# Kernel optimization log

Hardware: AMD Instinct MI355X
Metric: run time of the kernel (lower is better)

Reference implementation:

```python
import jax, jax.numpy as jnp
import numpy as np

A, B, NB = 100_000, 200_000, 6      # atoms, directed bonds, max neighbors
FA, FB, H = 133, 147, 256            # atom fdim, bond fdim, hidden
M, DEPTH = 5_000, 4                  # molecules, message-passing depth


def setup_inputs() -> dict:
    key = jax.random.key(0)
    ks = jax.random.split(key, 12)
    f_atoms = jax.random.normal(ks[0], (A, FA), jnp.float32)
    f_bonds = jax.random.normal(ks[1], (B, FB), jnp.float32)
    a2b = jax.random.randint(ks[2], (A, NB), 0, B, dtype=jnp.int32)
    b2a = jax.random.randint(ks[3], (B,), 0, A, dtype=jnp.int32)
    b2revb = jax.random.randint(ks[4], (B,), 0, B, dtype=jnp.int32)
    # weights (bias=False per args.bias, except W_o which always has bias)
    W_ia = jax.random.normal(ks[5], (FA, H), jnp.float32) / np.sqrt(FA)
    W_ib = jax.random.normal(ks[6], (FB, H), jnp.float32) / np.sqrt(FB)
    W_h = jax.random.normal(ks[7], (DEPTH - 1, H, H), jnp.float32) / np.sqrt(H)
    W_o = jax.random.normal(ks[8], (H, H), jnp.float32) / np.sqrt(H)
    b_o = jax.random.normal(ks[9], (H,), jnp.float32) * 0.01
    W_lr = jax.random.normal(ks[10], (3 * H, H), jnp.float32) / np.sqrt(3 * H)
    # ragged molecule sizes summing exactly to A (avg 20 atoms/mol)
    rng = np.random.default_rng(0)
    sizes = (A // M) + rng.integers(-5, 6, M)
    sizes[-1] += A - sizes.sum()
    sizes = jnp.asarray(sizes, jnp.int32)
    return dict(f_atoms=f_atoms, f_bonds=f_bonds, W_ia=W_ia, W_ib=W_ib,
                W_h=W_h, W_o=W_o, b_o=b_o, W_lr=W_lr,
                a2b=a2b, b2a=b2a, b2revb=b2revb, sizes=sizes)


def _sum_max_agg(message_bond, a2b):
    nei = message_bond[a2b]                 # [A, NB, H] gather
    return nei.sum(axis=1) * nei.max(axis=1)


def reference(f_atoms, f_bonds, W_ia, W_ib, W_h, W_o, b_o, W_lr,
              a2b, b2a, b2revb, sizes):
    input_atom = jax.nn.relu(f_atoms @ W_ia)    # [A, H]
    message_atom = input_atom
    input_bond = jax.nn.relu(f_bonds @ W_ib)    # [B, H]
    message_bond = input_bond
    for d in range(DEPTH - 1):
        agg = _sum_max_agg(message_bond, a2b)          # [A, H]
        message_atom = message_atom + agg
        rev = message_bond[b2revb]                     # [B, H]
        message_bond = message_atom[b2a] - rev
        message_bond = jax.nn.relu(input_bond + message_bond @ W_h[d])
        # dropout p=0.0 -> identity
    agg = _sum_max_agg(message_bond, a2b)              # [A, H]
    agg = jnp.concatenate([agg, message_atom, input_atom], axis=1) @ W_lr
    atom_hiddens = jax.nn.relu(agg @ W_o + b_o)        # [A, H]
    # ragged per-molecule mean pooling (a_scope)
    mol_ids = jnp.repeat(jnp.arange(M), sizes, total_repeat_length=A)
    sums = jax.ops.segment_sum(atom_hiddens, mol_ids, num_segments=M)
    mol_vecs = sums / sizes[:, None].astype(atom_hiddens.dtype)
    return mol_vecs                                    # [M, H]
```

## Files before the change

kernel.cpp:

```cpp
#include <hip/hip_runtime.h>


typedef _Float16 f16;
typedef f16 f16x4 __attribute__((ext_vector_type(4)));
typedef __attribute__((ext_vector_type(8))) short bh8;
typedef __attribute__((ext_vector_type(4))) float f32x4;

#define MB_SCALE 0.000244140625f
#define MB_INV   4096.0f
#define AGG_INV  16777216.0f

__device__ __forceinline__ unsigned short f2bf_rne(float f) {
    unsigned u = __float_as_uint(f);
    unsigned r = (u + 0x7fffu + ((u >> 16) & 1u)) >> 16;
    return (unsigned short)r;
}
__device__ __forceinline__ float bfu2f(unsigned short u) {
    return __uint_as_float(((unsigned)u) << 16);
}
__device__ __forceinline__ f32x4 mfma16(bh8 a, bh8 b, f32x4 c) {
    return __builtin_amdgcn_mfma_f32_16x16x32_bf16(a, b, c, 0, 0, 0);
}

__global__ __launch_bounds__(256) void wprep_kernel(
    const float* __restrict__ Wia, const float* __restrict__ Wib,
    const float* __restrict__ Wh,  const float* __restrict__ Wlr,
    const float* __restrict__ Wo,  short* __restrict__ ws)
{
    short* WiaT_hi = ws;
    short* WiaT_lo = ws + 40960;
    short* WibT_hi = ws + 81920;
    short* WibT_lo = ws + 122880;
    short* WhT_hi  = ws + 163840;
    short* WhT_lo  = ws + 360448;
    short* WlrT_hi = ws + 557056;
    short* WlrT_lo = ws + 753664;
    short* WoT_hi  = ws + 950272;
    short* WoT_lo  = ws + 1015808;

    int idx = blockIdx.x * 256 + threadIdx.x;
    float v; short *ph, *pl; int o;
    if (idx < 40960) {
        int n = idx / 160, k = idx - n * 160;
        v = (k < 133) ? Wia[(size_t)k * 256 + n] : 0.f;
        ph = WiaT_hi; pl = WiaT_lo; o = idx;
    } else if (idx < 81920) {
        int j = idx - 40960;
        int n = j / 160, k = j - n * 160;
        v = (k < 147) ? Wib[(size_t)k * 256 + n] : 0.f;
        ph = WibT_hi; pl = WibT_lo; o = j;
    } else if (idx < 278528) {
        int j = idx - 81920;
        int d = j >> 16, rem = j & 65535, n = rem >> 8, k = rem & 255;
        v = Wh[(size_t)d * 65536 + (size_t)k * 256 + n];
        ph = WhT_hi; pl = WhT_lo; o = j;
    } else if (idx < 475136) {
        int j = idx - 278528;
        int n = j / 768, k = j - n * 768;
        v = Wlr[(size_t)k * 256 + n];
        ph = WlrT_hi; pl = WlrT_lo; o = j;
    } else if (idx < 540672) {
        int j = idx - 475136;
        int n = j >> 8, k = j & 255;
        v = Wo[(size_t)k * 256 + n];
        ph = WoT_hi; pl = WoT_lo; o = j;
    } else return;
    unsigned short hb = f2bf_rne(v);
    ph[o] = (short)hb;
    pl[o] = (short)f2bf_rne(v - bfu2f(hb));
}

template <int KPAD, int SRC, int EPI>
__global__ __launch_bounds__(256) void mfma_gemm(
    const void* __restrict__ a0, const void* __restrict__ a1,
    const void* __restrict__ a2,
    const short* __restrict__ Bhi, const short* __restrict__ Blo,
    const float* __restrict__ bias, void* __restrict__ outv,
    int M, int Kact)
{
    __shared__ short As_hi[128 * 40];
    __shared__ short As_lo[(SRC == 2) ? 8 : 128 * 40];

    const int tid  = threadIdx.x;
    const int lane = tid & 63;
    const int w    = tid >> 6;
    const int wm   = (w >> 1) * 64;
    const int wn   = (w & 1) * 64;
    const int row0 = blockIdx.x * 128;
    const int colb = blockIdx.y * 128;

    const int sm = tid >> 1;
    const int sk = (tid & 1) * 16;
    const int fm = lane & 15;
    const int fk = (lane >> 4) * 8;

    int grow = row0 + sm; if (grow > M - 1) grow = M - 1;

    f32x4 acc[4][4];
#pragma unroll
    for (int i = 0; i < 4; ++i)
#pragma unroll
        for (int j = 0; j < 4; ++j) {
            f32x4 z = {0.f, 0.f, 0.f, 0.f};
            acc[i][j] = z;
        }

    for (int k0 = 0; k0 < KPAD; k0 += 32) {
        __syncthreads();
        if (SRC == 0) {
            const float* xrow = (const float*)a0 + (size_t)grow * Kact;
            bh8 h0, h1, l0, l1;
#pragma unroll
            for (int j = 0; j < 8; ++j) {
                int kc = k0 + sk + j;
                float v = (kc < Kact) ? xrow[kc] : 0.f;
                unsigned short hb = f2bf_rne(v);
                h0[j] = (short)hb; l0[j] = (short)f2bf_rne(v - bfu2f(hb));
                int kc2 = kc + 8;
                float v2 = (kc2 < Kact) ? xrow[kc2] : 0.f;
                unsigned short hb2 = f2bf_rne(v2);
                h1[j] = (short)hb2; l1[j] = (short)f2bf_rne(v2 - bfu2f(hb2));
            }
            int base = sm * 40 + sk;
            *(bh8*)&As_hi[base] = h0; *(bh8*)&As_hi[base + 8] = h1;
            *(bh8*)&As_lo[base] = l0; *(bh8*)&As_lo[base + 8] = l1;
        } else if (SRC == 1) {
            int base = sm * 40 + sk;
            if (k0 < 512) {
                const float* src = (k0 < 256) ? (const float*)a0 : (const float*)a1;
                int kl = k0 & 255;
                const float4* p = (const float4*)(src + (size_t)grow * 256 + kl + sk);
                float va[16];
#pragma unroll
                for (int q = 0; q < 4; ++q) {
                    float4 f = p[q];
                    va[q * 4 + 0] = f.x; va[q * 4 + 1] = f.y;
                    va[q * 4 + 2] = f.z; va[q * 4 + 3] = f.w;
                }
                bh8 h0, h1, l0, l1;
#pragma unroll
                for (int j = 0; j < 8; ++j) {
                    unsigned short hb = f2bf_rne(va[j]);
                    h0[j] = (short)hb; l0[j] = (short)f2bf_rne(va[j] - bfu2f(hb));
                    unsigned short hb2 = f2bf_rne(va[8 + j]);
                    h1[j] = (short)hb2; l1[j] = (short)f2bf_rne(va[8 + j] - bfu2f(hb2));
                }
                *(bh8*)&As_hi[base] = h0; *(bh8*)&As_hi[base + 8] = h1;
                *(bh8*)&As_lo[base] = l0; *(bh8*)&As_lo[base + 8] = l1;
            } else {
                const short* ia = (const short*)a2 + (size_t)grow * 256 + (k0 - 512) + sk;
                bh8 z;
#pragma unroll
                for (int j = 0; j < 8; ++j) z[j] = 0;
                *(bh8*)&As_hi[base]     = *(const bh8*)ia;
                *(bh8*)&As_hi[base + 8] = *(const bh8*)(ia + 8);
                *(bh8*)&As_lo[base] = z; *(bh8*)&As_lo[base + 8] = z;
            }
        } else {
            const short* xr = (const short*)a0 + (size_t)grow * 256 + k0 + sk;
            int base = sm * 40 + sk;
            *(bh8*)&As_hi[base]     = *(const bh8*)xr;
            *(bh8*)&As_hi[base + 8] = *(const bh8*)(xr + 8);
        }
        __syncthreads();

        bh8 bhf[4], blf[4];
#pragma unroll
        for (int nt = 0; nt < 4; ++nt) {
            int n = colb + wn + nt * 16 + fm;
            size_t off = (size_t)n * KPAD + k0 + fk;
            bhf[nt] = *(const bh8*)(Bhi + off);
            blf[nt] = *(const bh8*)(Blo + off);
        }
#pragma unroll
        for (int mt = 0; mt < 4; ++mt) {
            int abase = (wm + mt * 16 + fm) * 40 + fk;
            bh8 ah = *(const bh8*)&As_hi[abase];
#pragma unroll
            for (int nt = 0; nt < 4; ++nt) {
                acc[mt][nt] = mfma16(ah, bhf[nt], acc[mt][nt]);
                acc[mt][nt] = mfma16(ah, blf[nt], acc[mt][nt]);
            }
            if (SRC != 2) {
                bh8 al = *(const bh8*)&As_lo[abase];
#pragma unroll
                for (int nt = 0; nt < 4; ++nt)
                    acc[mt][nt] = mfma16(al, bhf[nt], acc[mt][nt]);
            }
        }
    }

#pragma unroll
    for (int mt = 0; mt < 4; ++mt) {
        int rbase = row0 + wm + mt * 16 + (lane >> 4) * 4;
#pragma unroll
        for (int nt = 0; nt < 4; ++nt) {
            int col = colb + wn + nt * 16 + fm;
            float bc = (EPI == 4) ? bias[col] : 0.f;
#pragma unroll
            for (int r = 0; r < 4; ++r) {
                int row = rbase + r;
                if (row < M) {
                    size_t o = (size_t)row * 256 + col;
                    float v = acc[mt][nt][r];
                    if (EPI == 0)      ((float*)outv)[o] = fmaxf(v, 0.f);
                    else if (EPI == 1) ((unsigned short*)outv)[o] = f2bf_rne(fmaxf(v, 0.f));
                    else if (EPI == 2) ((f16*)outv)[o] = (f16)(fmaxf(v, 0.f) * MB_SCALE);
                    else if (EPI == 3) ((unsigned short*)outv)[o] = f2bf_rne(v);
                    else               ((float*)outv)[o] = fmaxf(v + bc, 0.f);
                }
            }
        }
    }
}

__global__ __launch_bounds__(256) void bond_mfma_kernel(
    const float* __restrict__ FB,
    const short* __restrict__ WibT_hi, const short* __restrict__ WibT_lo,
    const short* __restrict__ WhT_hi,  const short* __restrict__ WhT_lo,
    const float* __restrict__ matom, const f16* __restrict__ mb_old,
    const int* __restrict__ b2a, const int* __restrict__ b2revb,
    f16* __restrict__ mb_new, int M)
{
    __shared__ short As_hi[128 * 40];
    __shared__ short As_lo[128 * 40];

    const int tid  = threadIdx.x;
    const int lane = tid & 63;
    const int w    = tid >> 6;
    const int wm   = (w >> 1) * 64;
    const int wn   = (w & 1) * 64;
    const int row0 = blockIdx.x * 128;
    const int colb = blockIdx.y * 128;

    const int sm = tid >> 1;
    const int sk = (tid & 1) * 16;

    int grow = row0 + sm; if (grow > M - 1) grow = M - 1;
    const float* frow = FB + (size_t)grow * 147;
    const float* arow = matom + (size_t)b2a[grow] * 256;
    const f16*   rrow = mb_old + (size_t)b2revb[grow] * 256;

    const int fm = lane & 15;
    const int fk = (lane >> 4) * 8;

    f32x4 acc[4][4];
#pragma unroll
    for (int i = 0; i < 4; ++i)
#pragma unroll
        for (int j = 0; j < 4; ++j) {
            f32x4 z = {0.f, 0.f, 0.f, 0.f};
            acc[i][j] = z;
        }

    for (int k0 = 0; k0 < 160; k0 += 32) {
        __syncthreads();
        {
            bh8 h0, h1, l0, l1;
#pragma unroll
            for (int j = 0; j < 8; ++j) {
                int kc = k0 + sk + j;
                float v = (kc < 147) ? frow[kc] : 0.f;
                unsigned short hb = f2bf_rne(v);
                h0[j] = (short)hb; l0[j] = (short)f2bf_rne(v - bfu2f(hb));
                int kc2 = kc + 8;
                float v2 = (kc2 < 147) ? frow[kc2] : 0.f;
                unsigned short hb2 = f2bf_rne(v2);
                h1[j] = (short)hb2; l1[j] = (short)f2bf_rne(v2 - bfu2f(hb2));
            }
            int base = sm * 40 + sk;
            *(bh8*)&As_hi[base] = h0; *(bh8*)&As_hi[base + 8] = h1;
            *(bh8*)&As_lo[base] = l0; *(bh8*)&As_lo[base + 8] = l1;
        }
        __syncthreads();

        bh8 bhf[4], blf[4];
#pragma unroll
        for (int nt = 0; nt < 4; ++nt) {
            int n = colb + wn + nt * 16 + fm;
            size_t off = (size_t)n * 160 + k0 + fk;
            bhf[nt] = *(const bh8*)(WibT_hi + off);
            blf[nt] = *(const bh8*)(WibT_lo + off);
        }
#pragma unroll
        for (int mt = 0; mt < 4; ++mt) {
            int abase = (wm + mt * 16 + fm) * 40 + fk;
            bh8 ah = *(const bh8*)&As_hi[abase];
            bh8 al = *(const bh8*)&As_lo[abase];
#pragma unroll
            for (int nt = 0; nt < 4; ++nt) {
                acc[mt][nt] = mfma16(ah, bhf[nt], acc[mt][nt]);
                acc[mt][nt] = mfma16(ah, blf[nt], acc[mt][nt]);
                acc[mt][nt] = mfma16(al, bhf[nt], acc[mt][nt]);
            }
        }
    }

#pragma unroll
    for (int i = 0; i < 4; ++i)
#pragma unroll
        for (int j = 0; j < 4; ++j)
#pragma unroll
            for (int r = 0; r < 4; ++r)
                acc[i][j][r] = fmaxf(acc[i][j][r], 0.f);

    for (int k0 = 0; k0 < 256; k0 += 32) {
        __syncthreads();
        {
            float va[16];
            const float4* ap = (const float4*)(arow + k0 + sk);
            const f16x4*  rp = (const f16x4*)(rrow + k0 + sk);
#pragma unroll
            for (int q = 0; q < 4; ++q) {
                float4 a = ap[q]; f16x4 r = rp[q];
                va[q * 4 + 0] = fmaf(-MB_INV, (float)r[0], a.x);
                va[q * 4 + 1] = fmaf(-MB_INV, (float)r[1], a.y);
                va[q * 4 + 2] = fmaf(-MB_INV, (float)r[2], a.z);
                va[q * 4 + 3] = fmaf(-MB_INV, (float)r[3], a.w);
            }
            bh8 h0, h1, l0, l1;
#pragma unroll
            for (int j = 0; j < 8; ++j) {
                unsigned short hb = f2bf_rne(va[j]);
                h0[j] = (short)hb; l0[j] = (short)f2bf_rne(va[j] - bfu2f(hb));
                unsigned short hb2 = f2bf_rne(va[8 + j]);
                h1[j] = (short)hb2; l1[j] = (short)f2bf_rne(va[8 + j] - bfu2f(hb2));
            }
            int base = sm * 40 + sk;
            *(bh8*)&As_hi[base] = h0; *(bh8*)&As_hi[base + 8] = h1;
            *(bh8*)&As_lo[base] = l0; *(bh8*)&As_lo[base + 8] = l1;
        }
        __syncthreads();

        bh8 bhf[4], blf[4];
#pragma unroll
        for (int nt = 0; nt < 4; ++nt) {
            int n = colb + wn + nt * 16 + fm;
            size_t off = (size_t)n * 256 + k0 + fk;
            bhf[nt] = *(const bh8*)(WhT_hi + off);
            blf[nt] = *(const bh8*)(WhT_lo + off);
        }
#pragma unroll
        for (int mt = 0; mt < 4; ++mt) {
            int abase = (wm + mt * 16 + fm) * 40 + fk;
            bh8 ah = *(const bh8*)&As_hi[abase];
            bh8 al = *(const bh8*)&As_lo[abase];
#pragma unroll
            for (int nt = 0; nt < 4; ++nt) {
                acc[mt][nt] = mfma16(ah, bhf[nt], acc[mt][nt]);
                acc[mt][nt] = mfma16(ah, blf[nt], acc[mt][nt]);
                acc[mt][nt] = mfma16(al, bhf[nt], acc[mt][nt]);
            }
        }
    }

#pragma unroll
    for (int mt = 0; mt < 4; ++mt) {
        int rbase = row0 + wm + mt * 16 + (lane >> 4) * 4;
#pragma unroll
        for (int nt = 0; nt < 4; ++nt) {
            int col = colb + wn + nt * 16 + fm;
#pragma unroll
            for (int r = 0; r < 4; ++r) {
                int row = rbase + r;
                if (row < M)
                    mb_new[(size_t)row * 256 + col] =
                        (f16)(fmaxf(acc[mt][nt][r], 0.f) * MB_SCALE);
            }
        }
    }
}

__global__ __launch_bounds__(256) void agg_kernel(
    const f16* __restrict__ mb, const int* __restrict__ a2b,
    float* __restrict__ matom, float* __restrict__ agg_out, int A)
{
    const int a = blockIdx.x;
    const int h = threadIdx.x;
    const int* nb = a2b + (size_t)a * 6;
    int i0 = nb[0], i1 = nb[1], i2 = nb[2], i3 = nb[3], i4 = nb[4], i5 = nb[5];
    float v0 = (float)mb[(size_t)i0 * 256 + h];
    float v1 = (float)mb[(size_t)i1 * 256 + h];
    float v2 = (float)mb[(size_t)i2 * 256 + h];
    float v3 = (float)mb[(size_t)i3 * 256 + h];
    float v4 = (float)mb[(size_t)i4 * 256 + h];
    float v5 = (float)mb[(size_t)i5 * 256 + h];
    float s = v0 + v1 + v2 + v3 + v4 + v5;
    float mx = fmaxf(fmaxf(fmaxf(v0, v1), fmaxf(v2, v3)), fmaxf(v4, v5));
    float g = AGG_INV * s * mx;
    size_t idx = (size_t)a * 256 + h;
    if (agg_out) agg_out[idx] = g;
    else         matom[idx] += g;
}

__global__ __launch_bounds__(256) void scan_kernel(
    const int* __restrict__ sizes, int* __restrict__ offsets, int M)
{
    __shared__ int part[256];
    const int t = threadIdx.x;
    const int chunk = (M + 255) / 256;
    int begin = t * chunk;
    int end = begin + chunk; if (end > M) end = M;
    int s = 0;
    for (int i = begin; i < end && i < M; ++i) s += sizes[i];
    part[t] = s;
    __syncthreads();
    for (int off = 1; off < 256; off <<= 1) {
        int v = (t >= off) ? part[t - off] : 0;
        __syncthreads();
        part[t] += v;
        __syncthreads();
    }
    int run = part[t] - s;
    for (int i = begin; i < end && i < M; ++i) { offsets[i] = run; run += sizes[i]; }
}

__global__ __launch_bounds__(256) void pool_kernel(
    const float* __restrict__ hid, const int* __restrict__ offsets,
    const int* __restrict__ sizes, float* __restrict__ out, int M, int A)
{
    const int m = blockIdx.x;
    const int h = threadIdx.x;
    int e = offsets[m];
    int sz = sizes[m];
    int start = e < A ? e : A;          if (start < 0) start = 0;
    int stop  = e + sz; if (stop > A) stop = A; if (stop < 0) stop = 0;
    float s = 0.f;
    for (int i = start; i < stop; ++i)
        s += hid[(size_t)i * 256 + h];
    out[(size_t)m * 256 + h] = s / (float)sz;
}

extern "C" void kernel_launch(void* const* d_in, const int* in_sizes, int n_in,
                              void* d_out, int out_size, void* d_ws, size_t ws_size,
                              hipStream_t stream)
{
    const float* f_atoms = (const float*)d_in[0];
    const float* f_bonds = (const float*)d_in[1];
    const float* W_ia    = (const float*)d_in[2];
    const float* W_ib    = (const float*)d_in[3];
    const float* W_h     = (const float*)d_in[4];
    const float* W_o     = (const float*)d_in[5];
    const float* b_o     = (const float*)d_in[6];
    const float* W_lr    = (const float*)d_in[7];
    const int*   a2b     = (const int*)d_in[8];
    const int*   b2a     = (const int*)d_in[9];
    const int*   b2revb  = (const int*)d_in[10];
    const int*   sizes   = (const int*)d_in[11];
    float* out = (float*)d_out;

    const int An = 100000, Bn = 200000, Mm = 5000;
    const size_t ABYTES = (size_t)An * 256 * 4;
    const size_t BBYTES = (size_t)Bn * 256 * 2;

    int*   offsets = (int*)d_ws;
    float* matom   = (float*)((char*)d_ws + 32768);
    f16*   mb0     = (f16*)((char*)matom + ABYTES);
    f16*   mb1     = (f16*)((char*)mb0 + BBYTES);
    short* wsplit  = (short*)((char*)mb1 + BBYTES);

    short* WiaT_hi = wsplit;
    short* WiaT_lo = wsplit + 40960;
    short* WibT_hi = wsplit + 81920;
    short* WibT_lo = wsplit + 122880;
    short* WhT_hi  = wsplit + 163840;
    short* WhT_lo  = wsplit + 360448;
    short* WlrT_hi = wsplit + 557056;
    short* WlrT_lo = wsplit + 753664;
    short* WoT_hi  = wsplit + 950272;
    short* WoT_lo  = wsplit + 1015808;

    dim3 blk(256);
    dim3 gA((An + 127) / 128, 2);
    dim3 gB((Bn + 127) / 128, 2);

    wprep_kernel<<<2112, blk, 0, stream>>>(W_ia, W_ib, W_h, W_lr, W_o, wsplit);

    mfma_gemm<160, 0, 0><<<gA, blk, 0, stream>>>(
        f_atoms, nullptr, nullptr, WiaT_hi, WiaT_lo, nullptr, matom, An, 133);
    mfma_gemm<160, 0, 2><<<gB, blk, 0, stream>>>(
        f_bonds, nullptr, nullptr, WibT_hi, WibT_lo, nullptr, mb0, Bn, 147);

    f16* cur = mb0; f16* nxt = mb1;
    for (int d = 0; d < 3; ++d) {
        agg_kernel<<<An, blk, 0, stream>>>(cur, a2b, matom, (float*)nullptr, An);
        bond_mfma_kernel<<<gB, blk, 0, stream>>>(
            f_bonds, WibT_hi, WibT_lo,
            WhT_hi + (size_t)d * 65536, WhT_lo + (size_t)d * 65536,
            matom, cur, b2a, b2revb, nxt, Bn);
        f16* t = cur; cur = nxt; nxt = t;
    }

    float* aggbuf = (float*)mb0;
    agg_kernel<<<An, blk, 0, stream>>>(cur, a2b, matom, aggbuf, An);

    unsigned short* iatom = (unsigned short*)mb1;
    unsigned short* t1    = (unsigned short*)((char*)mb1 + 51200000);
    mfma_gemm<160, 0, 1><<<gA, blk, 0, stream>>>(
        f_atoms, nullptr, nullptr, WiaT_hi, WiaT_lo, nullptr, iatom, An, 133);

    mfma_gemm<768, 1, 3><<<gA, blk, 0, stream>>>(
        aggbuf, matom, iatom, WlrT_hi, WlrT_lo, nullptr, t1, An, 768);

    float* hid = (float*)mb0;
    mfma_gemm<256, 2, 4><<<gA, blk, 0, stream>>>(
        t1, nullptr, nullptr, WoT_hi, WoT_lo, b_o, hid, An, 256);

    scan_kernel<<<1, 256, 0, stream>>>(sizes, offsets, Mm);
    pool_kernel<<<Mm, blk, 0, stream>>>(hid, offsets, sizes, out, Mm, An);
}
```

Measured before the change: 2.250 ms.

## Widen GEMM tiles to full 256 columns, double-buffer bond kernel, vectorize aggregation

The GEMM and bond kernels now use 512-thread blocks, so each block covers all 256 output columns. The A-tile is loaded and split into bf16 hi/lo once per row block instead of once per column half, which removes the duplicated input reads and conversion work. The bond kernel merges its two K loops into one 13-stage loop with a double-buffered shared-memory pipeline, so global loads overlap the MFMA work. The aggregation kernel handles four atoms per block, with each lane loading four halves as a vector. The risks are higher register pressure under launch_bounds(512,4) and half as many blocks to spread across the CUs.

```diff
diff --git a/kernel.cpp b/kernel.cpp
--- a/kernel.cpp
+++ b/kernel.cpp
@@ -71,7 +71,7 @@
 }
 
 template <int KPAD, int SRC, int EPI>
-__global__ __launch_bounds__(256) void mfma_gemm(
+__global__ __launch_bounds__(512, 4) void mfma_gemm(
     const void* __restrict__ a0, const void* __restrict__ a1,
     const void* __restrict__ a2,
     const short* __restrict__ Bhi, const short* __restrict__ Blo,
@@ -84,13 +84,12 @@
     const int tid  = threadIdx.x;
     const int lane = tid & 63;
     const int w    = tid >> 6;
-    const int wm   = (w >> 1) * 64;
-    const int wn   = (w & 1) * 64;
+    const int wm   = (w >> 2) * 64;
+    const int wn   = (w & 3) * 64;
     const int row0 = blockIdx.x * 128;
-    const int colb = blockIdx.y * 128;
-
-    const int sm = tid >> 1;
-    const int sk = (tid & 1) * 16;
+
+    const int sm = tid >> 2;
+    const int sk = (tid & 3) * 8;
     const int fm = lane & 15;
     const int fk = (lane >> 4) * 8;
 
@@ -107,67 +106,57 @@
 
     for (int k0 = 0; k0 < KPAD; k0 += 32) {
         __syncthreads();
+        int base = sm * 40 + sk;
         if (SRC == 0) {
             const float* xrow = (const float*)a0 + (size_t)grow * Kact;
-            bh8 h0, h1, l0, l1;
+            bh8 h0, l0;
 #pragma unroll
             for (int j = 0; j < 8; ++j) {
                 int kc = k0 + sk + j;
                 float v = (kc < Kact) ? xrow[kc] : 0.f;
                 unsigned short hb = f2bf_rne(v);
                 h0[j] = (short)hb; l0[j] = (short)f2bf_rne(v - bfu2f(hb));
-                int kc2 = kc + 8;
-                float v2 = (kc2 < Kact) ? xrow[kc2] : 0.f;
-                unsigned short hb2 = f2bf_rne(v2);
-                h1[j] = (short)hb2; l1[j] = (short)f2bf_rne(v2 - bfu2f(hb2));
-            }
-            int base = sm * 40 + sk;
-            *(bh8*)&As_hi[base] = h0; *(bh8*)&As_hi[base + 8] = h1;
-            *(bh8*)&As_lo[base] = l0; *(bh8*)&As_lo[base + 8] = l1;
+            }
+            *(bh8*)&As_hi[base] = h0;
+            *(bh8*)&As_lo[base] = l0;
         } else if (SRC == 1) {
-            int base = sm * 40 + sk;
             if (k0 < 512) {
                 const float* src = (k0 < 256) ? (const float*)a0 : (const float*)a1;
                 int kl = k0 & 255;
                 const float4* p = (const float4*)(src + (size_t)grow * 256 + kl + sk);
-                float va[16];
-#pragma unroll
-                for (int q = 0; q < 4; ++q) {
+                float va[8];
+#pragma unroll
+                for (int q = 0; q < 2; ++q) {
                     float4 f = p[q];
                     va[q * 4 + 0] = f.x; va[q * 4 + 1] = f.y;
                     va[q * 4 + 2] = f.z; va[q * 4 + 3] = f.w;
                 }
-                bh8 h0, h1, l0, l1;
+                bh8 h0, l0;
 #pragma unroll
                 for (int j = 0; j < 8; ++j) {
                     unsigned short hb = f2bf_rne(va[j]);
                     h0[j] = (short)hb; l0[j] = (short)f2bf_rne(va[j] - bfu2f(hb));
-                    unsigned short hb2 = f2bf_rne(va[8 + j]);
-                    h1[j] = (short)hb2; l1[j] = (short)f2bf_rne(va[8 + j] - bfu2f(hb2));
                 }
-                *(bh8*)&As_hi[base] = h0; *(bh8*)&As_hi[base + 8] = h1;
-                *(bh8*)&As_lo[base] = l0; *(bh8*)&As_lo[base + 8] = l1;
+                *(bh8*)&As_hi[base] = h0;
+                *(bh8*)&As_lo[base] = l0;
             } else {
                 const short* ia = (const short*)a2 + (size_t)grow * 256 + (k0 - 512) + sk;
                 bh8 z;
 #pragma unroll
                 for (int j = 0; j < 8; ++j) z[j] = 0;
-                *(bh8*)&As_hi[base]     = *(const bh8*)ia;
-                *(bh8*)&As_hi[base + 8] = *(const bh8*)(ia + 8);
-                *(bh8*)&As_lo[base] = z; *(bh8*)&As_lo[base + 8] = z;
+                *(bh8*)&As_hi[base] = *(const bh8*)ia;
+                *(bh8*)&As_lo[base] = z;
             }
         } else {
             const short* xr = (const short*)a0 + (size_t)grow * 256 + k0 + sk;
-            int base = sm * 40 + sk;
-            *(bh8*)&As_hi[base]     = *(const bh8*)xr;
-            *(bh8*)&As_hi[base + 8] = *(const bh8*)(xr + 8);
+            *(bh8*)&As_hi[base] = *(const bh8*)xr;
         }
         __syncthreads();
 
         bh8 bhf[4], blf[4];
 #pragma unroll
         for (int nt = 0; nt < 4; ++nt) {
-            int n = colb + wn + nt * 16 + fm;
+            int n = wn + nt * 16 + fm;
             size_t off = (size_t)n * KPAD + k0 + fk;
             bhf[nt] = *(const bh8*)(Bhi + off);
             blf[nt] = *(const bh8*)(Blo + off);
@@ -195,7 +184,7 @@
         int rbase = row0 + wm + mt * 16 + (lane >> 4) * 4;
 #pragma unroll
         for (int nt = 0; nt < 4; ++nt) {
-            int col = colb + wn + nt * 16 + fm;
+            int col = wn + nt * 16 + fm;
             float bc = (EPI == 4) ? bias[col] : 0.f;
 #pragma unroll
             for (int r = 0; r < 4; ++r) {
@@ -214,7 +203,7 @@
     }
 }
 
-__global__ __launch_bounds__(256) void bond_mfma_kernel(
+__global__ __launch_bounds__(512, 4) void bond_mfma_kernel(
     const float* __restrict__ FB,
     const short* __restrict__ WibT_hi, const short* __restrict__ WibT_lo,
     const short* __restrict__ WhT_hi,  const short* __restrict__ WhT_lo,
@@ -222,19 +211,17 @@
     const int* __restrict__ b2a, const int* __restrict__ b2revb,
     f16* __restrict__ mb_new, int M)
 {
-    __shared__ short As_hi[128 * 40];
-    __shared__ short As_lo[128 * 40];
+    __shared__ short As[2][2][128 * 40];
 
     const int tid  = threadIdx.x;
     const int lane = tid & 63;
     const int w    = tid >> 6;
-    const int wm   = (w >> 1) * 64;
-    const int wn   = (w & 1) * 64;
+    const int wm   = (w >> 2) * 64;
+    const int wn   = (w & 3) * 64;
     const int row0 = blockIdx.x * 128;
-    const int colb = blockIdx.y * 128;
-
-    const int sm = tid >> 1;
-    const int sk = (tid & 1) * 16;
+
+    const int sm = tid >> 2;
+    const int sk = (tid & 3) * 8;
 
     int grow = row0 + sm; if (grow > M - 1) grow = M - 1;
     const float* frow = FB + (size_t)grow * 147;
@@ -253,98 +240,59 @@
             acc[i][j] = z;
         }
 
-    for (int k0 = 0; k0 < 160; k0 += 32) {
-        __syncthreads();
-        {
-            bh8 h0, h1, l0, l1;
+    float va[8];
+
+    auto load = [&](int s) {
+        if (s < 5) {
+            int kb = s * 32 + sk;
 #pragma unroll
             for (int j = 0; j < 8; ++j) {
-                int kc = k0 + sk + j;
-                float v = (kc < 147) ? frow[kc] : 0.f;
-                unsigned short hb = f2bf_rne(v);
-                h0[j] = (short)hb; l0[j] = (short)f2bf_rne(v - bfu2f(hb));
-                int kc2 = kc + 8;
-                float v2 = (kc2 < 147) ? frow[kc2] : 0.f;
-                unsigned short hb2 = f2bf_rne(v2);
-                h1[j] = (short)hb2; l1[j] = (short)f2bf_rne(v2 - bfu2f(hb2));
-            }
-            int base = sm * 40 + sk;
-            *(bh8*)&As_hi[base] = h0; *(bh8*)&As_hi[base + 8] = h1;
-            *(bh8*)&As_lo[base] = l0; *(bh8*)&As_lo[base + 8] = l1;
-        }
-        __syncthreads();
-
-        bh8 bhf[4], blf[4];
-#pragma unroll
-        for (int nt = 0; nt < 4; ++nt) {
-            int n = colb + wn + nt * 16 + fm;
-            size_t off = (size_t)n * 160 + k0 + fk;
-            bhf[nt] = *(const bh8*)(WibT_hi + off);
-            blf[nt] = *(const bh8*)(WibT_lo + off);
-        }
-#pragma unroll
-        for (int mt = 0; mt < 4; ++mt) {
-            int abase = (wm + mt * 16 + fm) * 40 + fk;
-            bh8 ah = *(const bh8*)&As_hi[abase];
-            bh8 al = *(const bh8*)&As_lo[abase];
-#pragma unroll
-            for (int nt = 0; nt < 4; ++nt) {
-                acc[mt][nt] = mfma16(ah, bhf[nt], acc[mt][nt]);
-                acc[mt][nt] = mfma16(ah, blf[nt], acc[mt][nt]);
-                acc[mt][nt] = mfma16(al, bhf[nt], acc[mt][nt]);
-            }
-        }
-    }
-
-#pragma unroll
-    for (int i = 0; i < 4; ++i)
-#pragma unroll
-        for (int j = 0; j < 4; ++j)
-#pragma unroll
-            for (int r = 0; r < 4; ++r)
-                acc[i][j][r] = fmaxf(acc[i][j][r], 0.f);
-
-    for (int k0 = 0; k0 < 256; k0 += 32) {
-        __syncthreads();
-        {
-            float va[16];
-            const float4* ap = (const float4*)(arow + k0 + sk);
-            const f16x4*  rp = (const f16x4*)(rrow + k0 + sk);
-#pragma unroll
-            for (int q = 0; q < 4; ++q) {
+                int kc = kb + j;
+                va[j] = (kc < 147) ? frow[kc] : 0.f;
+            }
+        } else {
+            int kb = (s - 5) * 32 + sk;
+            const float4* ap = (const float4*)(arow + kb);
+            const f16x4*  rp = (const f16x4*)(rrow + kb);
+#pragma unroll
+            for (int q = 0; q < 2; ++q) {
                 float4 a = ap[q]; f16x4 r = rp[q];
                 va[q * 4 + 0] = fmaf(-MB_INV, (float)r[0], a.x);
                 va[q * 4 + 1] = fmaf(-MB_INV, (float)r[1], a.y);
                 va[q * 4 + 2] = fmaf(-MB_INV, (float)r[2], a.z);
                 va[q * 4 + 3] = fmaf(-MB_INV, (float)r[3], a.w);
             }
-            bh8 h0, h1, l0, l1;
-#pragma unroll
-            for (int j = 0; j < 8; ++j) {
-                unsigned short hb = f2bf_rne(va[j]);
-                h0[j] = (short)hb; l0[j] = (short)f2bf_rne(va[j] - bfu2f(hb));
-                unsigned short hb2 = f2bf_rne(va[8 + j]);
-                h1[j] = (short)hb2; l1[j] = (short)f2bf_rne(va[8 + j] - bfu2f(hb2));
-            }
-            int base = sm * 40 + sk;
-            *(bh8*)&As_hi[base] = h0; *(bh8*)&As_hi[base + 8] = h1;
-            *(bh8*)&As_lo[base] = l0; *(bh8*)&As_lo[base + 8] = l1;
-        }
-        __syncthreads();
-
+        }
+    };
+    auto store = [&](int buf) {
+        bh8 h, l;
+#pragma unroll
+        for (int j = 0; j < 8; ++j) {
+            unsigned short hb = f2bf_rne(va[j]);
+            h[j] = (short)hb;
+            l[j] = (short)f2bf_rne(va[j] - bfu2f(hb));
+        }
+        int base = sm * 40 + sk;
+        *(bh8*)&As[buf][0][base] = h;
+        *(bh8*)&As[buf][1][base] = l;
+    };
+    auto compute = [&](int buf, int s) {
+        const short *Bh, *Bl; int ldb, k0;
+        if (s < 5) { Bh = WibT_hi; Bl = WibT_lo; ldb = 160; k0 = s * 32; }
+        else       { Bh = WhT_hi;  Bl = WhT_lo;  ldb = 256; k0 = (s - 5) * 32; }
         bh8 bhf[4], blf[4];
 #pragma unroll
         for (int nt = 0; nt < 4; ++nt) {
-            int n = colb + wn + nt * 16 + fm;
-            size_t off = (size_t)n * 256 + k0 + fk;
-            bhf[nt] = *(const bh8*)(WhT_hi + off);
-            blf[nt] = *(const bh8*)(WhT_lo + off);
+            int n = wn + nt * 16 + fm;
+            size_t off = (size_t)n * ldb + k0 + fk;
+            bhf[nt] = *(const bh8*)(Bh + off);
+            blf[nt] = *(const bh8*)(Bl + off);
         }
 #pragma unroll
         for (int mt = 0; mt < 4; ++mt) {
             int abase = (wm + mt * 16 + fm) * 40 + fk;
-            bh8 ah = *(const bh8*)&As_hi[abase];
-            bh8 al = *(const bh8*)&As_lo[abase];
+            bh8 ah = *(const bh8*)&As[buf][0][abase];
+            bh8 al = *(const bh8*)&As[buf][1][abase];
 #pragma unroll
             for (int nt = 0; nt < 4; ++nt) {
                 acc[mt][nt] = mfma16(ah, bhf[nt], acc[mt][nt]);
@@ -352,6 +300,28 @@
                 acc[mt][nt] = mfma16(al, bhf[nt], acc[mt][nt]);
             }
         }
+    };
+
+    load(0);
+    store(0);
+    __syncthreads();
+
+    int cur = 0;
+    for (int s = 0; s < 13; ++s) {
+        if (s < 12) load(s + 1);
+        compute(cur, s);
+        if (s == 4) {
+#pragma unroll
+            for (int i = 0; i < 4; ++i)
+#pragma unroll
+                for (int j = 0; j < 4; ++j)
+#pragma unroll
+                    for (int r = 0; r < 4; ++r)
+                        acc[i][j][r] = fmaxf(acc[i][j][r], 0.f);
+        }
+        if (s < 12) store(cur ^ 1);
+        __syncthreads();
+        cur ^= 1;
     }
 
 #pragma unroll
@@ -359,7 +329,7 @@
         int rbase = row0 + wm + mt * 16 + (lane >> 4) * 4;
 #pragma unroll
         for (int nt = 0; nt < 4; ++nt) {
-            int col = colb + wn + nt * 16 + fm;
+            int col = wn + nt * 16 + fm;
 #pragma unroll
             for (int r = 0; r < 4; ++r) {
                 int row = rbase + r;
@@ -375,22 +345,33 @@
     const f16* __restrict__ mb, const int* __restrict__ a2b,
     float* __restrict__ matom, float* __restrict__ agg_out, int A)
 {
-    const int a = blockIdx.x;
-    const int h = threadIdx.x;
+    const int a    = blockIdx.x * 4 + (threadIdx.x >> 6);
+    const int lane = threadIdx.x & 63;
+    if (a >= A) return;
     const int* nb = a2b + (size_t)a * 6;
-    int i0 = nb[0], i1 = nb[1], i2 = nb[2], i3 = nb[3], i4 = nb[4], i5 = nb[5];
-    float v0 = (float)mb[(size_t)i0 * 256 + h];
-    float v1 = (float)mb[(size_t)i1 * 256 + h];
-    float v2 = (float)mb[(size_t)i2 * 256 + h];
-    float v3 = (float)mb[(size_t)i3 * 256 + h];
-    float v4 = (float)mb[(size_t)i4 * 256 + h];
-    float v5 = (float)mb[(size_t)i5 * 256 + h];
-    float s = v0 + v1 + v2 + v3 + v4 + v5;
-    float mx = fmaxf(fmaxf(fmaxf(v0, v1), fmaxf(v2, v3)), fmaxf(v4, v5));
-    float g = AGG_INV * s * mx;
-    size_t idx = (size_t)a * 256 + h;
-    if (agg_out) agg_out[idx] = g;
-    else         matom[idx] += g;
+
+    f16x4 v0 = *(const f16x4*)(mb + (size_t)nb[0] * 256 + lane * 4);
+    float s0 = (float)v0[0], s1 = (float)v0[1], s2 = (float)v0[2], s3 = (float)v0[3];
+    float m0 = s0, m1 = s1, m2 = s2, m3 = s3;
+#pragma unroll
+    for (int j = 1; j < 6; ++j) {
+        f16x4 v = *(const f16x4*)(mb + (size_t)nb[j] * 256 + lane * 4);
+        float f0 = (float)v[0], f1 = (float)v[1], f2 = (float)v[2], f3 = (float)v[3];
+        s0 += f0; s1 += f1; s2 += f2; s3 += f3;
+        m0 = fmaxf(m0, f0); m1 = fmaxf(m1, f1);
+        m2 = fmaxf(m2, f2); m3 = fmaxf(m3, f3);
+    }
+    size_t o = (size_t)a * 256 + lane * 4;
+    if (agg_out) {
+        float4 g = { AGG_INV * s0 * m0, AGG_INV * s1 * m1,
+                     AGG_INV * s2 * m2, AGG_INV * s3 * m3 };
+        *(float4*)(agg_out + o) = g;
+    } else {
+        float4 m = *(const float4*)(matom + o);
+        m.x += AGG_INV * s0 * m0; m.y += AGG_INV * s1 * m1;
+        m.z += AGG_INV * s2 * m2; m.w += AGG_INV * s3 * m3;
+        *(float4*)(matom + o) = m;
+    }
 }
 
 __global__ __launch_bounds__(256) void scan_kernel(
@@ -471,20 +452,21 @@
     short* WoT_lo  = wsplit + 1015808;
 
     dim3 blk(256);
-    dim3 gA((An + 127) / 128, 2);
-    dim3 gB((Bn + 127) / 128, 2);
+    dim3 blk512(512);
+    dim3 gA((An + 127) / 128, 1);
+    dim3 gB((Bn + 127) / 128, 1);
 
     wprep_kernel<<<2112, blk, 0, stream>>>(W_ia, W_ib, W_h, W_lr, W_o, wsplit);
 
-    mfma_gemm<160, 0, 0><<<gA, blk, 0, stream>>>(
+    mfma_gemm<160, 0, 0><<<gA, blk512, 0, stream>>>(
         f_atoms, nullptr, nullptr, WiaT_hi, WiaT_lo, nullptr, matom, An, 133);
-    mfma_gemm<160, 0, 2><<<gB, blk, 0, stream>>>(
+    mfma_gemm<160, 0, 2><<<gB, blk512, 0, stream>>>(
         f_bonds, nullptr, nullptr, WibT_hi, WibT_lo, nullptr, mb0, Bn, 147);
 
     f16* cur = mb0; f16* nxt = mb1;
     for (int d = 0; d < 3; ++d) {
-        agg_kernel<<<An, blk, 0, stream>>>(cur, a2b, matom, (float*)nullptr, An);
-        bond_mfma_kernel<<<gB, blk, 0, stream>>>(
+        agg_kernel<<<(An + 3) / 4, blk, 0, stream>>>(cur, a2b, matom, (float*)nullptr, An);
+        bond_mfma_kernel<<<gB, blk512, 0, stream>>>(
             f_bonds, WibT_hi, WibT_lo,
             WhT_hi + (size_t)d * 65536, WhT_lo + (size_t)d * 65536,
             matom, cur, b2a, b2revb, nxt, Bn);
@@ -492,18 +474,18 @@
     }
 
     float* aggbuf = (float*)mb0;
-    agg_kernel<<<An, blk, 0, stream>>>(cur, a2b, matom, aggbuf, An);
+    agg_kernel<<<(An + 3) / 4, blk, 0, stream>>>(cur, a2b, matom, aggbuf, An);
 
     unsigned short* iatom = (unsigned short*)mb1;
     unsigned short* t1    = (unsigned short*)((char*)mb1 + 51200000);
-    mfma_gemm<160, 0, 1><<<gA, blk, 0, stream>>>(
+    mfma_gemm<160, 0, 1><<<gA, blk512, 0, stream>>>(
         f_atoms, nullptr, nullptr, WiaT_hi, WiaT_lo, nullptr, iatom, An, 133);
 
-    mfma_gemm<768, 1, 3><<<gA, blk, 0, stream>>>(
+    mfma_gemm<768, 1, 3><<<gA, blk512, 0, stream>>>(
         aggbuf, matom, iatom, WlrT_hi, WlrT_lo, nullptr, t1, An, 768);
 
     float* hid = (float*)mb0;
-    mfma_gemm<256, 2, 4><<<gA, blk, 0, stream>>>(
+    mfma_gemm<256, 2, 4><<<gA, blk512, 0, stream>>>(
         t1, nullptr, nullptr, WoT_hi, WoT_lo, b_o, hid, An, 256);
 
     scan_kernel<<<1, 256, 0, stream>>>(sizes, offsets, Mm);
```

Measured after the change: 1.923 ms. -14.5%, faster.
